# Kernel tuning notes

Hardware: AMD Instinct MI355X
Metric: run time of the kernel (lower is better)

The kernel has to match this reference:

```python
import jax, jax.numpy as jnp
import numpy as np

N = 30000      # paper nodes
E = 300000     # edges per etype
IN = 128       # in_feats
HID = 128      # n_hidden
H, D = 4, 32   # n_heads, head dim (HID // H)
C = 16         # n_classes
T = 2          # n_etypes
SLOPE = 0.2    # GATConv leaky-relu negative slope


def setup_inputs() -> dict:
    key = jax.random.key(0)
    ks = jax.random.split(key, 24)
    def w(k, shape, fan):
        return jax.random.normal(k, shape, jnp.float32) * (fan ** -0.5)
    inp = {}
    inp["x"] = jax.random.normal(ks[0], (N, IN), jnp.float32)
    inp["src0"] = jax.random.randint(ks[1], (E,), 0, N, jnp.int32)
    inp["dst0"] = jax.random.randint(ks[2], (E,), 0, N, jnp.int32)
    inp["src1"] = jax.random.randint(ks[3], (E,), 0, N, jnp.int32)
    inp["dst1"] = jax.random.randint(ks[4], (E,), 0, N, jnp.int32)
    # layer 1: in_feats -> H*D, per etype (stacked on leading etype axis)
    inp["W1"]  = w(ks[5], (T, IN, H * D), IN)
    inp["al1"] = w(ks[6], (T, H, D), D)
    inp["ar1"] = w(ks[7], (T, H, D), D)
    inp["b1"]  = jnp.zeros((T, H * D), jnp.float32)
    # layers 2,3: HID -> H*D
    inp["W2"]  = w(ks[8], (T, HID, H * D), HID)
    inp["al2"] = w(ks[9], (T, H, D), D)
    inp["ar2"] = w(ks[10], (T, H, D), D)
    inp["b2"]  = jnp.zeros((T, H * D), jnp.float32)
    inp["W3"]  = w(ks[11], (T, HID, H * D), HID)
    inp["al3"] = w(ks[12], (T, H, D), D)
    inp["ar3"] = w(ks[13], (T, H, D), D)
    inp["b3"]  = jnp.zeros((T, H * D), jnp.float32)
    # output linear
    inp["Wout"] = w(ks[14], (HID, C), HID)
    inp["bout"] = jnp.zeros((C,), jnp.float32)
    return inp


def _gat(h, src, dst, W, al, ar, b):
    """Single-etype GATConv. h:[N,F], W:[F,H*D], al/ar:[H,D], b:[H*D] -> [N,H,D]."""
    feat = (h @ W).reshape(N, H, D)                       # [N,H,D]
    el = jnp.sum(feat * al, axis=-1)                      # [N,H]
    er = jnp.sum(feat * ar, axis=-1)                      # [N,H]
    e = jax.nn.leaky_relu(el[src] + er[dst], SLOPE)       # [E,H]
    # edge softmax over incoming edges of each dst node, per head
    m = jax.ops.segment_max(e, dst, num_segments=N)       # [N,H]
    ex = jnp.exp(e - m[dst])                              # [E,H]
    s = jax.ops.segment_sum(ex, dst, num_segments=N)      # [N,H]
    alpha = ex / s[dst]                                   # [E,H]
    msg = feat[src] * alpha[:, :, None]                   # [E,H,D]
    out = jax.ops.segment_sum(msg, dst, num_segments=N)   # [N,H,D]
    return out + b.reshape(1, H, D)


def _hetero_layer(h, srcs, dsts, W, al, ar, b):
    # HeteroGraphConv: sum-aggregate GATConv outputs across etypes, then flatten heads
    out = _gat(h, srcs[0], dsts[0], W[0], al[0], ar[0], b[0])
    for t in range(1, T):
        out = out + _gat(h, srcs[t], dsts[t], W[t], al[t], ar[t], b[t])
    return out.reshape(N, H * D)


def reference(x, src0, dst0, src1, dst1,
              W1, al1, ar1, b1, W2, al2, ar2, b2, W3, al3, ar3, b3,
              Wout, bout):
    srcs, dsts = (src0, src1), (dst0, dst1)
    h = _hetero_layer(x, srcs, dsts, W1, al1, ar1, b1)
    h = jax.nn.relu(h)  # dropout omitted (eval mode)
    h = _hetero_layer(h, srcs, dsts, W2, al2, ar2, b2)
    h = jax.nn.relu(h)
    h = _hetero_layer(h, srcs, dsts, W3, al3, ar3, b3)
    return h @ Wout + bout  # [N, C]
```

## Files before the change

### kernel.cpp

```cpp
#include <hip/hip_runtime.h>

#define NN 30000
#define EE 300000
#define HH 4
#define SLOPE 0.2f
#define SCAN_NB 15

typedef _Float16 f16;
struct f16x2 { f16 x, y; };
typedef f16 f16x8 __attribute__((ext_vector_type(8)));
typedef float f32x4 __attribute__((ext_vector_type(4)));

__global__ __launch_bounds__(256) void zero_k(int4* __restrict__ p, int n4) {
    const int i = blockIdx.x * 256 + threadIdx.x;
    if (i < n4) p[i] = make_int4(0, 0, 0, 0);
}

__global__ __launch_bounds__(256) void wconv_k(const float* __restrict__ W,
                                               f16* __restrict__ Wh) {
    const int t = blockIdx.y;
    const int i0 = blockIdx.x * 2048;
    #pragma unroll
    for (int j = 0; j < 8; ++j) {
        const int i = i0 + threadIdx.x + j * 256;
        const int k = i >> 7, col = i & 127;
        Wh[t * 16384 + col * 128 + k] = (f16)W[t * 16384 + i];
    }
}

#define APAD 136
__global__ __launch_bounds__(256) void gemm_mfma(const float* __restrict__ A,
                                                 const f16* __restrict__ Whbase,
                                                 const float* __restrict__ albase,
                                                 const float* __restrict__ arbase,
                                                 f16* __restrict__ featbase,
                                                 float* __restrict__ elbase,
                                                 float* __restrict__ erbase) {
    __shared__ f16 Asl[64 * APAD];
    __shared__ f16 Bsl[128 * APAD];
    const int et = blockIdx.y;
    const f16* Wh = Whbase + et * 16384;
    f16* feat = featbase + (size_t)et * NN * 128;
    const int row0 = blockIdx.x * 64;
    const int t = threadIdx.x;

    #pragma unroll
    for (int j = 0; j < 8; ++j) {
        const int idx = t + j * 256;
        const int r = idx >> 5, q = idx & 31;
        const int row = row0 + r;
        float4 v = make_float4(0.f, 0.f, 0.f, 0.f);
        if (row < NN) v = reinterpret_cast<const float4*>(A)[row * 32 + q];
        union { f16 h[4]; float2 d; } pk;
        pk.h[0] = (f16)v.x; pk.h[1] = (f16)v.y; pk.h[2] = (f16)v.z; pk.h[3] = (f16)v.w;
        *reinterpret_cast<float2*>(&Asl[r * APAD + q * 4]) = pk.d;
    }
    #pragma unroll
    for (int j = 0; j < 8; ++j) {
        const int idx = t + j * 256;
        const int col = idx >> 4, k16 = idx & 15;
        *reinterpret_cast<float4*>(&Bsl[col * APAD + k16 * 8]) =
            *reinterpret_cast<const float4*>(Wh + col * 128 + k16 * 8);
    }
    __syncthreads();

    const int w = t >> 6, lane = t & 63;
    const int r = lane & 15, g = lane >> 4;
    const int mb = w * 16;
    f32x4 acc[8];
    #pragma unroll
    for (int nt = 0; nt < 8; ++nt) acc[nt] = (f32x4){0.f, 0.f, 0.f, 0.f};

    #pragma unroll
    for (int ks = 0; ks < 4; ++ks) {
        const f16x8 av = *reinterpret_cast<const f16x8*>(&Asl[(mb + r) * APAD + ks * 32 + g * 8]);
        #pragma unroll
        for (int nt = 0; nt < 8; ++nt) {
            const f16x8 bv =
                *reinterpret_cast<const f16x8*>(&Bsl[(nt * 16 + r) * APAD + ks * 32 + g * 8]);
            acc[nt] = __builtin_amdgcn_mfma_f32_16x16x32_f16(av, bv, acc[nt], 0, 0, 0);
        }
    }

    float alv[8], arv[8];
    #pragma unroll
    for (int nt = 0; nt < 8; ++nt) {
        alv[nt] = albase[et * 128 + nt * 16 + r];
        arv[nt] = arbase[et * 128 + nt * 16 + r];
    }
    #pragma unroll
    for (int p = 0; p < 4; ++p) {
        const int row = row0 + mb + g * 4 + p;
        const bool ok = row < NN;
        if (ok) {
            #pragma unroll
            for (int nt = 0; nt < 8; ++nt)
                feat[(size_t)row * 128 + nt * 16 + r] = (f16)acc[nt][p];
        }
        #pragma unroll
        for (int h = 0; h < 4; ++h) {
            float pl = fmaf(acc[2 * h][p], alv[2 * h], acc[2 * h + 1][p] * alv[2 * h + 1]);
            float pr = fmaf(acc[2 * h][p], arv[2 * h], acc[2 * h + 1][p] * arv[2 * h + 1]);
            pl += __shfl_xor(pl, 1); pl += __shfl_xor(pl, 2);
            pl += __shfl_xor(pl, 4); pl += __shfl_xor(pl, 8);
            pr += __shfl_xor(pr, 1); pr += __shfl_xor(pr, 2);
            pr += __shfl_xor(pr, 4); pr += __shfl_xor(pr, 8);
            if (ok && r == 0) {
                elbase[et * NN * HH + row * HH + h] = pl;
                erbase[et * NN * HH + row * HH + h] = pr;
            }
        }
    }
}

__global__ __launch_bounds__(256) void hist_k(const int* __restrict__ dst0,
                                              const int* __restrict__ dst1,
                                              int* __restrict__ deg) {
    const int e = blockIdx.x * 256 + threadIdx.x;
    if (e >= EE) return;
    const int t = blockIdx.y;
    const int* d = t ? dst1 : dst0;
    atomicAdd(&deg[t * NN + d[e]], 1);
}

__global__ __launch_bounds__(256) void scan1_k(const int* __restrict__ deg,
                                               int* __restrict__ offs,
                                               int* __restrict__ blocksum) {
    const int t = blockIdx.y, b = blockIdx.x;
    const int* d = deg + t * NN;
    int* o = offs + t * (NN + 1);
    const int base = b * 2048 + threadIdx.x * 8;
    int v[8];
    int s = 0;
    #pragma unroll
    for (int j = 0; j < 8; ++j) {
        const int i = base + j;
        v[j] = (i < NN) ? d[i] : 0;
        s += v[j];
    }
    __shared__ int buf[256];
    buf[threadIdx.x] = s;
    __syncthreads();
    #pragma unroll
    for (int ofs = 1; ofs < 256; ofs <<= 1) {
        const int add = (threadIdx.x >= (unsigned)ofs) ? buf[threadIdx.x - ofs] : 0;
        __syncthreads();
        buf[threadIdx.x] += add;
        __syncthreads();
    }
    int run = buf[threadIdx.x] - s;
    #pragma unroll
    for (int j = 0; j < 8; ++j) {
        const int i = base + j;
        if (i < NN) o[i] = run;
        run += v[j];
    }
    if (threadIdx.x == 255) blocksum[t * SCAN_NB + b] = buf[255];
}

__global__ __launch_bounds__(64) void scan2_k(int* __restrict__ blocksum,
                                              int* __restrict__ offs) {
    if (threadIdx.x != 0) return;
    #pragma unroll
    for (int t = 0; t < 2; ++t) {
        int run = 0;
        for (int b = 0; b < SCAN_NB; ++b) {
            const int v = blocksum[t * SCAN_NB + b];
            blocksum[t * SCAN_NB + b] = run;
            run += v;
        }
        offs[t * (NN + 1) + NN] = run;
    }
}

__global__ __launch_bounds__(256) void scan3_k(int* __restrict__ offs,
                                               const int* __restrict__ blocksum,
                                               int* __restrict__ cursor) {
    const int t = blockIdx.y, b = blockIdx.x;
    const int boff = blocksum[t * SCAN_NB + b];
    int* o = offs + t * (NN + 1);
    int* cur = cursor + t * NN;
    const int base = b * 2048 + threadIdx.x * 8;
    #pragma unroll
    for (int j = 0; j < 8; ++j) {
        const int i = base + j;
        if (i < NN) {
            const int val = o[i] + boff;
            o[i] = val;
            cur[i] = val;
        }
    }
}

__global__ __launch_bounds__(256) void scatter_k(const int* __restrict__ src0,
                                                 const int* __restrict__ dst0,
                                                 const int* __restrict__ src1,
                                                 const int* __restrict__ dst1,
                                                 int* __restrict__ cursor,
                                                 int* __restrict__ csr_src) {
    const int e = blockIdx.x * 256 + threadIdx.x;
    if (e >= EE) return;
    const int t = blockIdx.y;
    const int* s = t ? src1 : src0;
    const int* d = t ? dst1 : dst0;
    const int pos = atomicAdd(&cursor[t * NN + d[e]], 1);
    csr_src[t * EE + pos] = s[e];
}

__global__ __launch_bounds__(256) void pull_agg_k(const int* __restrict__ csr_src,
                                                  const int* __restrict__ offs,
                                                  const float* __restrict__ el,
                                                  const float* __restrict__ er,
                                                  const f16* __restrict__ feat,
                                                  const float* __restrict__ b0,
                                                  const float* __restrict__ b1,
                                                  float* __restrict__ out, int relu) {
    const int wave = (blockIdx.x * 256 + threadIdx.x) >> 6;
    const int lane = threadIdx.x & 63;
    if (wave >= NN) return;
    const int n = wave;
    const int c0 = lane * 2;
    const int h = c0 >> 5;
    float a0 = 0.f, a1 = 0.f;
    #pragma unroll
    for (int t = 0; t < 2; ++t) {
        const int* so = offs + t * (NN + 1);
        const int e0 = so[n], e1 = so[n + 1];
        const float erh = er[t * NN * HH + n * HH + h];
        const int* cs = csr_src + t * EE;
        const f16* ft = feat + (size_t)t * NN * 128;
        const float* elt = el + t * NN * HH;
        float sA = 0.f, x0A = 0.f, x1A = 0.f;
        float sB = 0.f, x0B = 0.f, x1B = 0.f;
        float sC = 0.f, x0C = 0.f, x1C = 0.f;
        float sD = 0.f, x0D = 0.f, x1D = 0.f;
        int e = e0;
        for (; e + 3 < e1; e += 4) {
            const int sa = cs[e], sb = cs[e + 1], sc = cs[e + 2], sd = cs[e + 3];
            float va = elt[sa * HH + h] + erh;
            float vb = elt[sb * HH + h] + erh;
            float vc = elt[sc * HH + h] + erh;
            float vd = elt[sd * HH + h] + erh;
            const f16x2 fa = *reinterpret_cast<const f16x2*>(ft + (size_t)sa * 128 + c0);
            const f16x2 fb = *reinterpret_cast<const f16x2*>(ft + (size_t)sb * 128 + c0);
            const f16x2 fc = *reinterpret_cast<const f16x2*>(ft + (size_t)sc * 128 + c0);
            const f16x2 fd = *reinterpret_cast<const f16x2*>(ft + (size_t)sd * 128 + c0);
            va = (va >= 0.f) ? va : va * SLOPE;
            vb = (vb >= 0.f) ? vb : vb * SLOPE;
            vc = (vc >= 0.f) ? vc : vc * SLOPE;
            vd = (vd >= 0.f) ? vd : vd * SLOPE;
            const float ea = __expf(va), eb = __expf(vb);
            const float ec = __expf(vc), ed = __expf(vd);
            sA += ea; x0A = fmaf(ea, (float)fa.x, x0A); x1A = fmaf(ea, (float)fa.y, x1A);
            sB += eb; x0B = fmaf(eb, (float)fb.x, x0B); x1B = fmaf(eb, (float)fb.y, x1B);
            sC += ec; x0C = fmaf(ec, (float)fc.x, x0C); x1C = fmaf(ec, (float)fc.y, x1C);
            sD += ed; x0D = fmaf(ed, (float)fd.x, x0D); x1D = fmaf(ed, (float)fd.y, x1D);
        }
        for (; e < e1; ++e) {
            const int sa = cs[e];
            float va = elt[sa * HH + h] + erh;
            va = (va >= 0.f) ? va : va * SLOPE;
            const float ea = __expf(va);
            const f16x2 fa = *reinterpret_cast<const f16x2*>(ft + (size_t)sa * 128 + c0);
            sA += ea; x0A = fmaf(ea, (float)fa.x, x0A); x1A = fmaf(ea, (float)fa.y, x1A);
        }
        const float s = (sA + sB) + (sC + sD);
        const float x0 = (x0A + x0B) + (x0C + x0D);
        const float x1 = (x1A + x1B) + (x1C + x1D);
        const float inv = (s > 0.f) ? 1.f / s : 0.f;
        a0 = fmaf(x0, inv, a0);
        a1 = fmaf(x1, inv, a1);
    }
    a0 += b0[c0] + b1[c0];
    a1 += b0[c0 + 1] + b1[c0 + 1];
    if (relu) { a0 = fmaxf(a0, 0.f); a1 = fmaxf(a1, 0.f); }
    *reinterpret_cast<float2*>(out + (size_t)n * 128 + c0) = make_float2(a0, a1);
}

__global__ __launch_bounds__(256) void out_gemm_k(const float* __restrict__ A,
                                                  const float* __restrict__ W,
                                                  const float* __restrict__ bout,
                                                  float* __restrict__ out) {
    __shared__ float At[16][132];
    const int row0 = blockIdx.x * 16;
    const int t = threadIdx.x;
    for (int i = t; i < 16 * 32; i += 256) {
        const int r = i >> 5, c4 = i & 31;
        *reinterpret_cast<float4*>(&At[r][c4 * 4]) =
            reinterpret_cast<const float4*>(A)[(row0 + r) * 32 + c4];
    }
    __syncthreads();
    const int r = t >> 4, c = t & 15;
    float accv = 0.f;
    #pragma unroll 8
    for (int k = 0; k < 128; ++k) accv = fmaf(At[r][k], W[k * 16 + c], accv);
    out[(row0 + r) * 16 + c] = accv + bout[c];
}

extern "C" void kernel_launch(void* const* d_in, const int* in_sizes, int n_in,
                              void* d_out, int out_size, void* d_ws, size_t ws_size,
                              hipStream_t stream) {
    (void)in_sizes; (void)n_in; (void)out_size; (void)ws_size;
    const float* x = (const float*)d_in[0];
    const int* src0 = (const int*)d_in[1];
    const int* dst0 = (const int*)d_in[2];
    const int* src1 = (const int*)d_in[3];
    const int* dst1 = (const int*)d_in[4];
    const float* W[3]  = {(const float*)d_in[5], (const float*)d_in[9],  (const float*)d_in[13]};
    const float* al[3] = {(const float*)d_in[6], (const float*)d_in[10], (const float*)d_in[14]};
    const float* ar[3] = {(const float*)d_in[7], (const float*)d_in[11], (const float*)d_in[15]};
    const float* bb[3] = {(const float*)d_in[8], (const float*)d_in[12], (const float*)d_in[16]};
    const float* Wout = (const float*)d_in[17];
    const float* bout = (const float*)d_in[18];
    float* outp = (float*)d_out;

    char* pb = (char*)d_ws;
    f16* feat   = (f16*)pb;    pb += (size_t)2 * NN * 128 * 2;
    float* hbuf = (float*)pb;  pb += (size_t)NN * 128 * 4;
    float* el   = (float*)pb;  pb += (size_t)2 * NN * HH * 4;
    float* er   = (float*)pb;  pb += (size_t)2 * NN * HH * 4;
    int* deg    = (int*)pb;    pb += (size_t)2 * NN * 4;
    int* cursor = (int*)pb;    pb += (size_t)2 * NN * 4;
    int* offs   = (int*)pb;    pb += (size_t)2 * (NN + 1) * 4;
    int* bsum   = (int*)pb;    pb += (size_t)2 * SCAN_NB * 4;
    f16* Wh     = (f16*)pb;    pb += (size_t)3 * 2 * 128 * 128 * 2;
    int* csr    = (int*)pb;    pb += (size_t)2 * EE * 4;

    zero_k<<<(2 * NN / 4 + 255) / 256, 256, 0, stream>>>((int4*)deg, 2 * NN / 4);
    hist_k<<<dim3((EE + 255) / 256, 2), 256, 0, stream>>>(dst0, dst1, deg);
    scan1_k<<<dim3(SCAN_NB, 2), 256, 0, stream>>>(deg, offs, bsum);
    scan2_k<<<1, 64, 0, stream>>>(bsum, offs);
    scan3_k<<<dim3(SCAN_NB, 2), 256, 0, stream>>>(offs, bsum, cursor);
    scatter_k<<<dim3((EE + 255) / 256, 2), 256, 0, stream>>>(src0, dst0, src1, dst1, cursor, csr);
    for (int l = 0; l < 3; ++l)
        wconv_k<<<dim3(8, 2), 256, 0, stream>>>(W[l], Wh + l * 2 * 16384);

    const float* hin = x;
    for (int l = 0; l < 3; ++l) {
        gemm_mfma<<<dim3((NN + 63) / 64, 2), 256, 0, stream>>>(hin, Wh + l * 2 * 16384,
                                                               al[l], ar[l], feat, el, er);
        pull_agg_k<<<NN / 4, 256, 0, stream>>>(csr, offs, el, er, feat,
                                               bb[l], bb[l] + 128, hbuf, (l < 2) ? 1 : 0);
        hin = hbuf;
    }
    out_gemm_k<<<NN / 16, 256, 0, stream>>>(hbuf, Wout, bout, outp);
}
```

Before: 271.5 us.

## Split aggregation per etype across waves and store hidden activations in fp16

The pull aggregation kernel now gives each etype of a node its own wave, so two waves per node run in parallel. Their normalized partial sums are combined through shared memory before bias, relu and the write. Hidden activations are stored as fp16 instead of fp32, which halves the GEMM input and output-GEMM read traffic. The input x is converted to fp16 once up front and the three weight-conversion launches are merged into one. The cost is an extra conversion kernel, a block barrier in the aggregation, and lower precision on the intermediate activations.

Result: no change. 266.3 us (-1.9%).

```diff
diff --git a/kernel.cpp b/kernel.cpp
--- a/kernel.cpp
+++ b/kernel.cpp
@@ -16,20 +16,35 @@
     if (i < n4) p[i] = make_int4(0, 0, 0, 0);
 }
 
-__global__ __launch_bounds__(256) void wconv_k(const float* __restrict__ W,
-                                               f16* __restrict__ Wh) {
-    const int t = blockIdx.y;
+__global__ __launch_bounds__(256) void xconv_k(const float* __restrict__ x,
+                                               f16* __restrict__ xh) {
+    const int i = blockIdx.x * 256 + threadIdx.x;
+    const float4 a = reinterpret_cast<const float4*>(x)[i * 2];
+    const float4 b = reinterpret_cast<const float4*>(x)[i * 2 + 1];
+    union { f16 h[8]; float4 f4; } pk;
+    pk.h[0] = (f16)a.x; pk.h[1] = (f16)a.y; pk.h[2] = (f16)a.z; pk.h[3] = (f16)a.w;
+    pk.h[4] = (f16)b.x; pk.h[5] = (f16)b.y; pk.h[6] = (f16)b.z; pk.h[7] = (f16)b.w;
+    reinterpret_cast<float4*>(xh)[i] = pk.f4;
+}
+
+__global__ __launch_bounds__(256) void wconv3_k(const float* __restrict__ W0,
+                                                const float* __restrict__ W1,
+                                                const float* __restrict__ W2,
+                                                f16* __restrict__ Wh) {
+    const int l = blockIdx.z, t = blockIdx.y;
+    const float* W = (l == 0) ? W0 : ((l == 1) ? W1 : W2);
+    f16* Whl = Wh + (size_t)l * 2 * 16384;
     const int i0 = blockIdx.x * 2048;
     #pragma unroll
     for (int j = 0; j < 8; ++j) {
         const int i = i0 + threadIdx.x + j * 256;
         const int k = i >> 7, col = i & 127;
-        Wh[t * 16384 + col * 128 + k] = (f16)W[t * 16384 + i];
+        Whl[t * 16384 + col * 128 + k] = (f16)W[t * 16384 + i];
     }
 }
 
 #define APAD 136
-__global__ __launch_bounds__(256) void gemm_mfma(const float* __restrict__ A,
+__global__ __launch_bounds__(256) void gemm_mfma(const f16* __restrict__ Ah,
                                                  const f16* __restrict__ Whbase,
                                                  const float* __restrict__ albase,
                                                  const float* __restrict__ arbase,
@@ -45,15 +60,13 @@
     const int t = threadIdx.x;
 
     #pragma unroll
-    for (int j = 0; j < 8; ++j) {
+    for (int j = 0; j < 4; ++j) {
         const int idx = t + j * 256;
-        const int r = idx >> 5, q = idx & 31;
+        const int r = idx >> 4, q = idx & 15;
         const int row = row0 + r;
         float4 v = make_float4(0.f, 0.f, 0.f, 0.f);
-        if (row < NN) v = reinterpret_cast<const float4*>(A)[row * 32 + q];
-        union { f16 h[4]; float2 d; } pk;
-        pk.h[0] = (f16)v.x; pk.h[1] = (f16)v.y; pk.h[2] = (f16)v.z; pk.h[3] = (f16)v.w;
-        *reinterpret_cast<float2*>(&Asl[r * APAD + q * 4]) = pk.d;
+        if (row < NN) v = reinterpret_cast<const float4*>(Ah + (size_t)row * 128)[q];
+        *reinterpret_cast<float4*>(&Asl[r * APAD + q * 8]) = v;
     }
     #pragma unroll
     for (int j = 0; j < 8; ++j) {
@@ -207,87 +220,87 @@
     csr_src[t * EE + pos] = s[e];
 }
 
-__global__ __launch_bounds__(256) void pull_agg_k(const int* __restrict__ csr_src,
-                                                  const int* __restrict__ offs,
-                                                  const float* __restrict__ el,
-                                                  const float* __restrict__ er,
-                                                  const f16* __restrict__ feat,
-                                                  const float* __restrict__ b0,
-                                                  const float* __restrict__ b1,
-                                                  float* __restrict__ out, int relu) {
-    const int wave = (blockIdx.x * 256 + threadIdx.x) >> 6;
-    const int lane = threadIdx.x & 63;
-    if (wave >= NN) return;
-    const int n = wave;
+__global__ __launch_bounds__(256) void pull_agg2_k(const int* __restrict__ csr_src,
+                                                   const int* __restrict__ offs,
+                                                   const float* __restrict__ el,
+                                                   const float* __restrict__ er,
+                                                   const f16* __restrict__ feat,
+                                                   const float* __restrict__ b0,
+                                                   const float* __restrict__ b1,
+                                                   f16* __restrict__ out, int relu) {
+    __shared__ float xb[2][2][128];
+    const int w = threadIdx.x >> 6, lane = threadIdx.x & 63;
+    const int p = w >> 1, t = w & 1;
+    const int n = blockIdx.x * 2 + p;
     const int c0 = lane * 2;
     const int h = c0 >> 5;
-    float a0 = 0.f, a1 = 0.f;
-    #pragma unroll
-    for (int t = 0; t < 2; ++t) {
-        const int* so = offs + t * (NN + 1);
-        const int e0 = so[n], e1 = so[n + 1];
-        const float erh = er[t * NN * HH + n * HH + h];
-        const int* cs = csr_src + t * EE;
-        const f16* ft = feat + (size_t)t * NN * 128;
-        const float* elt = el + t * NN * HH;
-        float sA = 0.f, x0A = 0.f, x1A = 0.f;
-        float sB = 0.f, x0B = 0.f, x1B = 0.f;
-        float sC = 0.f, x0C = 0.f, x1C = 0.f;
-        float sD = 0.f, x0D = 0.f, x1D = 0.f;
-        int e = e0;
-        for (; e + 3 < e1; e += 4) {
-            const int sa = cs[e], sb = cs[e + 1], sc = cs[e + 2], sd = cs[e + 3];
-            float va = elt[sa * HH + h] + erh;
-            float vb = elt[sb * HH + h] + erh;
-            float vc = elt[sc * HH + h] + erh;
-            float vd = elt[sd * HH + h] + erh;
-            const f16x2 fa = *reinterpret_cast<const f16x2*>(ft + (size_t)sa * 128 + c0);
-            const f16x2 fb = *reinterpret_cast<const f16x2*>(ft + (size_t)sb * 128 + c0);
-            const f16x2 fc = *reinterpret_cast<const f16x2*>(ft + (size_t)sc * 128 + c0);
-            const f16x2 fd = *reinterpret_cast<const f16x2*>(ft + (size_t)sd * 128 + c0);
-            va = (va >= 0.f) ? va : va * SLOPE;
-            vb = (vb >= 0.f) ? vb : vb * SLOPE;
-            vc = (vc >= 0.f) ? vc : vc * SLOPE;
-            vd = (vd >= 0.f) ? vd : vd * SLOPE;
-            const float ea = __expf(va), eb = __expf(vb);
-            const float ec = __expf(vc), ed = __expf(vd);
-            sA += ea; x0A = fmaf(ea, (float)fa.x, x0A); x1A = fmaf(ea, (float)fa.y, x1A);
-            sB += eb; x0B = fmaf(eb, (float)fb.x, x0B); x1B = fmaf(eb, (float)fb.y, x1B);
-            sC += ec; x0C = fmaf(ec, (float)fc.x, x0C); x1C = fmaf(ec, (float)fc.y, x1C);
-            sD += ed; x0D = fmaf(ed, (float)fd.x, x0D); x1D = fmaf(ed, (float)fd.y, x1D);
-        }
-        for (; e < e1; ++e) {
-            const int sa = cs[e];
-            float va = elt[sa * HH + h] + erh;
-            va = (va >= 0.f) ? va : va * SLOPE;
-            const float ea = __expf(va);
-            const f16x2 fa = *reinterpret_cast<const f16x2*>(ft + (size_t)sa * 128 + c0);
-            sA += ea; x0A = fmaf(ea, (float)fa.x, x0A); x1A = fmaf(ea, (float)fa.y, x1A);
-        }
-        const float s = (sA + sB) + (sC + sD);
-        const float x0 = (x0A + x0B) + (x0C + x0D);
-        const float x1 = (x1A + x1B) + (x1C + x1D);
-        const float inv = (s > 0.f) ? 1.f / s : 0.f;
-        a0 = fmaf(x0, inv, a0);
-        a1 = fmaf(x1, inv, a1);
-    }
-    a0 += b0[c0] + b1[c0];
-    a1 += b0[c0 + 1] + b1[c0 + 1];
-    if (relu) { a0 = fmaxf(a0, 0.f); a1 = fmaxf(a1, 0.f); }
-    *reinterpret_cast<float2*>(out + (size_t)n * 128 + c0) = make_float2(a0, a1);
-}
-
-__global__ __launch_bounds__(256) void out_gemm_k(const float* __restrict__ A,
+
+    const int* so = offs + t * (NN + 1);
+    const int e0 = so[n], e1 = so[n + 1];
+    const float erh = er[t * NN * HH + n * HH + h];
+    const int* cs = csr_src + t * EE;
+    const f16* ft = feat + (size_t)t * NN * 128;
+    const float* elt = el + t * NN * HH;
+    float sA = 0.f, x0A = 0.f, x1A = 0.f;
+    float sB = 0.f, x0B = 0.f, x1B = 0.f;
+    float sC = 0.f, x0C = 0.f, x1C = 0.f;
+    float sD = 0.f, x0D = 0.f, x1D = 0.f;
+    int e = e0;
+    for (; e + 3 < e1; e += 4) {
+        const int sa = cs[e], sb = cs[e + 1], sc = cs[e + 2], sd = cs[e + 3];
+        float va = elt[sa * HH + h] + erh;
+        float vb = elt[sb * HH + h] + erh;
+        float vc = elt[sc * HH + h] + erh;
+        float vd = elt[sd * HH + h] + erh;
+        const f16x2 fa = *reinterpret_cast<const f16x2*>(ft + (size_t)sa * 128 + c0);
+        const f16x2 fb = *reinterpret_cast<const f16x2*>(ft + (size_t)sb * 128 + c0);
+        const f16x2 fc = *reinterpret_cast<const f16x2*>(ft + (size_t)sc * 128 + c0);
+        const f16x2 fd = *reinterpret_cast<const f16x2*>(ft + (size_t)sd * 128 + c0);
+        va = (va >= 0.f) ? va : va * SLOPE;
+        vb = (vb >= 0.f) ? vb : vb * SLOPE;
+        vc = (vc >= 0.f) ? vc : vc * SLOPE;
+        vd = (vd >= 0.f) ? vd : vd * SLOPE;
+        const float ea = __expf(va), eb = __expf(vb);
+        const float ec = __expf(vc), ed = __expf(vd);
+        sA += ea; x0A = fmaf(ea, (float)fa.x, x0A); x1A = fmaf(ea, (float)fa.y, x1A);
+        sB += eb; x0B = fmaf(eb, (float)fb.x, x0B); x1B = fmaf(eb, (float)fb.y, x1B);
+        sC += ec; x0C = fmaf(ec, (float)fc.x, x0C); x1C = fmaf(ec, (float)fc.y, x1C);
+        sD += ed; x0D = fmaf(ed, (float)fd.x, x0D); x1D = fmaf(ed, (float)fd.y, x1D);
+    }
+    for (; e < e1; ++e) {
+        const int sa = cs[e];
+        float va = elt[sa * HH + h] + erh;
+        va = (va >= 0.f) ? va : va * SLOPE;
+        const float ea = __expf(va);
+        const f16x2 fa = *reinterpret_cast<const f16x2*>(ft + (size_t)sa * 128 + c0);
+        sA += ea; x0A = fmaf(ea, (float)fa.x, x0A); x1A = fmaf(ea, (float)fa.y, x1A);
+    }
+    const float s = (sA + sB) + (sC + sD);
+    const float inv = (s > 0.f) ? 1.f / s : 0.f;
+    xb[p][t][c0]     = ((x0A + x0B) + (x0C + x0D)) * inv;
+    xb[p][t][c0 + 1] = ((x1A + x1B) + (x1C + x1D)) * inv;
+    __syncthreads();
+    if (t == 0) {
+        float a0 = xb[p][0][c0] + xb[p][1][c0] + b0[c0] + b1[c0];
+        float a1 = xb[p][0][c0 + 1] + xb[p][1][c0 + 1] + b0[c0 + 1] + b1[c0 + 1];
+        if (relu) { a0 = fmaxf(a0, 0.f); a1 = fmaxf(a1, 0.f); }
+        f16x2 o; o.x = (f16)a0; o.y = (f16)a1;
+        *reinterpret_cast<f16x2*>(out + (size_t)n * 128 + c0) = o;
+    }
+}
+
+__global__ __launch_bounds__(256) void out_gemm_k(const f16* __restrict__ A,
                                                   const float* __restrict__ W,
                                                   const float* __restrict__ bout,
                                                   float* __restrict__ out) {
     __shared__ float At[16][132];
     const int row0 = blockIdx.x * 16;
     const int t = threadIdx.x;
-    for (int i = t; i < 16 * 32; i += 256) {
-        const int r = i >> 5, c4 = i & 31;
-        *reinterpret_cast<float4*>(&At[r][c4 * 4]) =
-            reinterpret_cast<const float4*>(A)[(row0 + r) * 32 + c4];
+    {
+        const int r = t >> 4, c8 = t & 15;
+        const f16x8 v = *reinterpret_cast<const f16x8*>(A + (size_t)(row0 + r) * 128 + c8 * 8);
+        #pragma unroll
+        for (int j = 0; j < 8; ++j) At[r][c8 * 8 + j] = (float)v[j];
     }
     __syncthreads();
     const int r = t >> 4, c = t & 15;
@@ -316,7 +329,8 @@
 
     char* pb = (char*)d_ws;
     f16* feat   = (f16*)pb;    pb += (size_t)2 * NN * 128 * 2;
-    float* hbuf = (float*)pb;  pb += (size_t)NN * 128 * 4;
+    f16* xh     = (f16*)pb;    pb += (size_t)NN * 128 * 2;
+    f16* hbuf   = (f16*)pb;    pb += (size_t)NN * 128 * 2;
     float* el   = (float*)pb;  pb += (size_t)2 * NN * HH * 4;
     float* er   = (float*)pb;  pb += (size_t)2 * NN * HH * 4;
     int* deg    = (int*)pb;    pb += (size_t)2 * NN * 4;
@@ -332,15 +346,15 @@
     scan2_k<<<1, 64, 0, stream>>>(bsum, offs);
     scan3_k<<<dim3(SCAN_NB, 2), 256, 0, stream>>>(offs, bsum, cursor);
     scatter_k<<<dim3((EE + 255) / 256, 2), 256, 0, stream>>>(src0, dst0, src1, dst1, cursor, csr);
-    for (int l = 0; l < 3; ++l)
-        wconv_k<<<dim3(8, 2), 256, 0, stream>>>(W[l], Wh + l * 2 * 16384);
-
-    const float* hin = x;
+    wconv3_k<<<dim3(8, 2, 3), 256, 0, stream>>>(W[0], W[1], W[2], Wh);
+    xconv_k<<<NN * 128 / 8 / 256, 256, 0, stream>>>(x, xh);
+
+    const f16* hin = xh;
     for (int l = 0; l < 3; ++l) {
         gemm_mfma<<<dim3((NN + 63) / 64, 2), 256, 0, stream>>>(hin, Wh + l * 2 * 16384,
                                                                al[l], ar[l], feat, el, er);
-        pull_agg_k<<<NN / 4, 256, 0, stream>>>(csr, offs, el, er, feat,
-                                               bb[l], bb[l] + 128, hbuf, (l < 2) ? 1 : 0);
+        pull_agg2_k<<<NN / 2, 256, 0, stream>>>(csr, offs, el, er, feat,
+                                                bb[l], bb[l] + 128, hbuf, (l < 2) ? 1 : 0);
         hin = hbuf;
     }
     out_gemm_k<<<NN / 16, 256, 0, stream>>>(hbuf, Wout, bout, outp);
```
